# Kernel tuning notes

Hardware: AMD Instinct MI355X
Metric: run time of the kernel (lower is better)

Reference implementation:

```python
import jax, jax.numpy as jnp
from jax import lax
import numpy as np

B, C, T = 32, 62, 1024
SR = 256
NUM_T = 32
POOL, STEP = 16, 4
OUT_G, POOL_G = 64, 32
NUM_CLASS = 4
KS = [int(0.1 * SR), int(0.2 * SR), int(0.5 * SR)]  # 25, 51, 128
EPS = 1e-30

def _feat_size():
    total = 0
    for k in KS:
        L = T - k + 1
        total += (L - POOL) // STEP + 1
    return NUM_T * (total // 2)  # AvgPool(1,2) halves the concat length

F_DIM = _feat_size()  # 32 * 354 = 11328


def setup_inputs() -> dict:
    key = jax.random.key(0)
    ks = jax.random.split(key, 32)
    n = lambda i, shape, s=0.05: jax.random.normal(ks[i], shape, dtype=jnp.float32) * s
    return dict(
        x=jax.random.normal(ks[0], (B, 1, C, T), dtype=jnp.float32),
        conv1_w=n(1, (NUM_T, 1, 1, KS[0])), conv1_b=jnp.zeros((NUM_T,), jnp.float32),
        conv2_w=n(2, (NUM_T, 1, 1, KS[1])), conv2_b=jnp.zeros((NUM_T,), jnp.float32),
        conv3_w=n(3, (NUM_T, 1, 1, KS[2])), conv3_b=jnp.zeros((NUM_T,), jnp.float32),
        oxo_w=n(4, (NUM_T, NUM_T)), oxo_b=jnp.zeros((NUM_T,), jnp.float32),
        lf_w=n(5, (C, F_DIM), 1.0), lf_b=jnp.zeros((1, C, 1), jnp.float32),
        global_adj=n(6, (C, C), 1.0),
        entry_w=n(7, (F_DIM, OUT_G)), entry_b=jnp.zeros((1, 1, OUT_G), jnp.float32),
        pool_w=n(8, (F_DIM, POOL_G)), pool_b=jnp.zeros((1, 1, POOL_G), jnp.float32),
        pl_w=n(9, (POOL_G, POOL_G), 0.1), pl_b=jnp.zeros((POOL_G,), jnp.float32),
        embed_w=n(10, (OUT_G, OUT_G), 0.1), embed_b=jnp.zeros((1, 1, OUT_G), jnp.float32),
        fc1_w=n(11, (2 * OUT_G, 2 * OUT_G), 0.1), fc1_b=jnp.zeros((2 * OUT_G,), jnp.float32),
        fc2_w=n(12, (2 * OUT_G, OUT_G), 0.1), fc2_b=jnp.zeros((OUT_G,), jnp.float32),
        fc3_w=n(13, (OUT_G, NUM_CLASS), 0.1), fc3_b=jnp.zeros((NUM_CLASS,), jnp.float32),
    )


def _bn(t, axes, eps=1e-5):
    # training-mode batchnorm with gamma=1, beta=0 (init values)
    m = t.mean(axes, keepdims=True)
    v = t.var(axes, keepdims=True)
    return (t - m) / jnp.sqrt(v + eps)


def _temporal(x, w, b):
    # Conv2d(1, NUM_T, (1,k)) -> square -> AvgPool(1,POOL) stride (1,STEP) -> log
    y = lax.conv_general_dilated(x, w, (1, 1), 'VALID',
                                 dimension_numbers=('NCHW', 'OIHW', 'NCHW'))
    y = y + b[None, :, None, None]
    y = y * y
    y = lax.reduce_window(y, 0.0, lax.add, (1, 1, 1, POOL), (1, 1, 1, STEP), 'VALID') / POOL
    return jnp.log(y)


def _forward(x, conv1_w, conv1_b, conv2_w, conv2_b, conv3_w, conv3_b, oxo_w, oxo_b,
             lf_w, lf_b, global_adj, entry_w, entry_b, pool_w, pool_b, pl_w, pl_b,
             embed_w, embed_b, fc1_w, fc1_b, fc2_w, fc2_b, fc3_w, fc3_b):
    # temporal branches, concat along time
    out = jnp.concatenate([_temporal(x, conv1_w, conv1_b),
                           _temporal(x, conv2_w, conv2_b),
                           _temporal(x, conv3_w, conv3_b)], axis=-1)  # [B,NUM_T,C,Lt]
    out = _bn(out, (0, 2, 3))  # BN_t
    # OneXOneConv: dropout(eval)=id, 1x1 conv, leaky_relu, AvgPool(1,2)
    out = jnp.einsum('bchw,oc->bohw', out, oxo_w) + oxo_b[None, :, None, None]
    out = jnp.where(out > 0, out, 0.01 * out)
    out = lax.reduce_window(out, 0.0, lax.add, (1, 1, 1, 2), (1, 1, 1, 2), 'VALID') / 2.0
    out = _bn(out, (0, 2, 3))  # BN_t_
    # [B,NUM_T,C,L] -> [B,C,NUM_T*L]
    out = jnp.transpose(out, (0, 2, 1, 3)).reshape(out.shape[0], C, -1)
    # local_filter_fun + apply_bn
    out = jax.nn.relu(out * lf_w[None] - lf_b)
    out = _bn(out, (0, 2))
    # get_adj: self-similarity, learned global adj, self loops, sym normalization
    s = jnp.einsum('bnf,bmf->bnm', out, out)
    adj = jax.nn.relu(s * (global_adj + global_adj.T)) + jnp.eye(C, dtype=out.dtype)
    rowsum = adj.sum(-1)
    rowsum = jnp.where(rowsum == 0, rowsum + 1.0, rowsum)
    d = rowsum ** -0.5
    adj = adj * d[:, :, None] * d[:, None, :]
    # entry GCN + bn_ + attention pooling (softmax over last dim of size 1 -> ones)
    h_entry = _bn(jnp.einsum('bnm,bmf->bnf', adj, out) @ entry_w - entry_b, (0, 2))
    tg1 = jnp.tanh(h_entry.mean(1))
    sc1 = jax.nn.softmax(jnp.einsum('bnf,bf->bn', h_entry, tg1)[..., None], axis=-1)
    rep1 = jnp.einsum('bnf,bn->bf', h_entry, sc1[..., 0])
    # pool GCN -> assignment
    h_pool = _bn(jnp.einsum('bnm,bmf->bnf', adj, out) @ pool_w - pool_b, (0, 2))
    s_assign = jax.nn.softmax(h_pool @ pl_w + pl_b, axis=-1)  # [B,C,POOL_G]
    # dense_diff_pool
    x_pool = jnp.einsum('bnk,bnf->bkf', s_assign, h_entry)
    adj_pool = jnp.einsum('bnk,bnm,bml->bkl', s_assign, adj, s_assign)
    link = adj - jnp.einsum('bnk,bmk->bnm', s_assign, s_assign) + EPS
    link_loss = jnp.linalg.norm(link.reshape(-1)) / adj.size
    ent_loss = (-s_assign * jnp.log(s_assign + EPS)).sum(-1).mean()
    # embed GCN + apply_bn + attention pooling
    h = _bn(jnp.einsum('bkl,blf->bkf', adj_pool, x_pool) @ embed_w - embed_b, (0, 2))
    tg2 = jnp.tanh(h.mean(1))
    sc2 = jax.nn.softmax(jnp.einsum('bkf,bf->bk', h, tg2)[..., None], axis=-1)
    rep2 = jnp.einsum('bkf,bk->bf', h, sc2[..., 0])
    # head
    o = jnp.concatenate([rep1, rep2], axis=1)
    o = jax.nn.relu(o @ fc1_w + fc1_b)
    o = jax.nn.relu(o @ fc2_w + fc2_b)
    o = o @ fc3_w + fc3_b
    o = _bn(o, (0,))  # apply_bn on [B, num_class]
    return o, link_loss, ent_loss


def reference(x, conv1_w, conv1_b, conv2_w, conv2_b, conv3_w, conv3_b, oxo_w, oxo_b,
              lf_w, lf_b, global_adj, entry_w, entry_b, pool_w, pool_b, pl_w, pl_b,
              embed_w, embed_b, fc1_w, fc1_b, fc2_w, fc2_b, fc3_w, fc3_b):
    return _forward(x, conv1_w, conv1_b, conv2_w, conv2_b, conv3_w, conv3_b, oxo_w, oxo_b,
                    lf_w, lf_b, global_adj, entry_w, entry_b, pool_w, pool_b, pl_w, pl_b,
                    embed_w, embed_b, fc1_w, fc1_b, fc2_w, fc2_b, fc3_w, fc3_b)
```

## Files before the change

kernel.cpp:

```cpp
#include <hip/hip_runtime.h>
#include <math.h>

typedef float  f32x4 __attribute__((ext_vector_type(4)));
typedef short  s16x4 __attribute__((ext_vector_type(4)));
typedef short  s16x8 __attribute__((ext_vector_type(8)));

constexpr int cB  = 32;
constexpr int cC  = 62;
constexpr int cT  = 1024;
constexpr int cNT = 32;
constexpr int cLT = 708;
constexpr int cLT2= 354;
constexpr int cFD = 11328;
constexpr int cNBC = cB*cC;

constexpr size_t FEAT_N = (size_t)cB*cNT*cC*cLT;
constexpr size_t P_N    = (size_t)cB*cC*cC;
constexpr size_t Q_N    = (size_t)cB*cC*96;
constexpr size_t R_N    = (size_t)cB*64;
constexpr size_t PART_N = (size_t)cNBC*64;
constexpr size_t ADJ_N  = P_N;
constexpr size_t HE_N   = (size_t)cB*cC*64;
constexpr size_t HP_N   = (size_t)cB*cC*32;
constexpr size_t HPRE_N = (size_t)cB*32*64;
constexpr int WBF_N = 32*32 + 32*64 + 32*128;

__device__ __forceinline__ unsigned short bf16rne(float v){
  unsigned int u = __float_as_uint(v);
  unsigned int r = (u + 0x7fffu + ((u>>16)&1u)) >> 16;
  return (unsigned short)r;
}

__global__ __launch_bounds__(256) void k_prep(
    const float* __restrict__ w1, const float* __restrict__ w2,
    const float* __restrict__ w3, const float* __restrict__ entry_w,
    const float* __restrict__ pool_w,
    unsigned short* __restrict__ wH, unsigned short* __restrict__ wL,
    float* __restrict__ wcol)
{
  int blk = blockIdx.x, tid = threadIdx.x;
  if (blk < 28){
    int i = blk*256 + tid;
    float v;
    if (i < 1024){ int f=i>>5, k=i&31; v = (k<25) ? w1[f*25+k] : 0.f; }
    else if (i < 3072){ int j=i-1024; int f=j>>6, k=j&63; v = (k<51) ? w2[f*51+k] : 0.f; }
    else { v = w3[i-3072]; }
    unsigned short h = bf16rne(v);
    float hf = __uint_as_float(((unsigned int)h)<<16);
    wH[i] = h;
    wL[i] = bf16rne(v - hf);
  } else {
    int j = blk - 28;
    float s = 0.f;
    if (j < 64){ for (int k=tid;k<cFD;k+=256) s += entry_w[(size_t)k*64 + j]; }
    else       { for (int k=tid;k<cFD;k+=256) s += pool_w[(size_t)k*32 + (j-64)]; }
    __shared__ float red[256];
    red[tid]=s; __syncthreads();
    for (int o=128;o>0;o>>=1){ if(tid<o) red[tid]+=red[tid+o]; __syncthreads(); }
    if (tid==0) wcol[j] = red[0];
  }
}

template<int KS, int MT, int WOFF>
__device__ __forceinline__ void mfma_branch(
    const unsigned short* xH, const unsigned short* xL,
    const unsigned short* __restrict__ wHg, const unsigned short* __restrict__ wLg,
    const float* __restrict__ biasg, float* pt, int tid)
{
  int lane = tid & 63, wv = tid >> 6;
  int f = lane & 15, q = lane >> 4;
  int s = lane & 3;
  int a12 = lane & 12;
  s16x8 BH[2][KS], BL[2][KS];
  #pragma unroll
  for (int nt=0; nt<2; nt++)
    #pragma unroll
    for (int ks=0; ks<KS; ks++){
      size_t wo = (size_t)WOFF + (size_t)(nt*16+f)*(KS*32) + ks*32 + q*8;
      BH[nt][ks] = *(const s16x8*)&wHg[wo];
      BL[nt][ks] = *(const s16x8*)&wLg[wo];
    }
  float bv0 = biasg[f], bv1 = biasg[16+f];
  for (int mt = wv; mt < MT; mt += 4){
    f32x4 acc0 = {0.f,0.f,0.f,0.f};
    f32x4 acc1 = {0.f,0.f,0.f,0.f};
    int e0 = mt*16 + a12;
    #pragma unroll
    for (int ks=0; ks<KS; ks++){
      int e = e0 + q*8 + ks*32;
      const unsigned short* ph = xH + s*1160 + e;
      const unsigned short* pl = xL + s*1160 + e;
      s16x4 h0 = *(const s16x4*)ph;
      s16x4 h1 = *(const s16x4*)(ph+4);
      s16x4 l0 = *(const s16x4*)pl;
      s16x4 l1 = *(const s16x4*)(pl+4);
      s16x8 Ah = __builtin_shufflevector(h0,h1,0,1,2,3,4,5,6,7);
      s16x8 Al = __builtin_shufflevector(l0,l1,0,1,2,3,4,5,6,7);
      acc0 = __builtin_amdgcn_mfma_f32_16x16x32_bf16(Ah, BH[0][ks], acc0, 0,0,0);
      acc0 = __builtin_amdgcn_mfma_f32_16x16x32_bf16(Ah, BL[0][ks], acc0, 0,0,0);
      acc0 = __builtin_amdgcn_mfma_f32_16x16x32_bf16(Al, BH[0][ks], acc0, 0,0,0);
      acc1 = __builtin_amdgcn_mfma_f32_16x16x32_bf16(Ah, BH[1][ks], acc1, 0,0,0);
      acc1 = __builtin_amdgcn_mfma_f32_16x16x32_bf16(Ah, BL[1][ks], acc1, 0,0,0);
      acc1 = __builtin_amdgcn_mfma_f32_16x16x32_bf16(Al, BH[1][ks], acc1, 0,0,0);
    }
    float p0=0.f, p1=0.f;
    #pragma unroll
    for (int r=0;r<4;r++){
      float t0 = acc0[r]+bv0; p0 = fmaf(t0,t0,p0);
      float t1 = acc1[r]+bv1; p1 = fmaf(t1,t1,p1);
    }
    pt[(size_t)f*261      + mt*4 + q] = p0;
    pt[(size_t)(16+f)*261 + mt*4 + q] = p1;
  }
}

template<int P, int OFF>
__device__ __forceinline__ void pool_phase(
    const float* pt, float* __restrict__ feat, size_t rstr, size_t base_bc,
    float* tsum, float* tsq, int tid)
{
  bool act = tid < P;
  for (int fi=0; fi<32; fi++){
    float lv = 0.f;
    if (act){
      const float* pp = &pt[(size_t)fi*261 + tid];
      float pooled = (pp[0]+pp[1]+pp[2]+pp[3])*(1.f/16.f);
      lv = __logf(pooled);
      feat[base_bc + (size_t)fi*rstr + OFF + tid] = lv;
    }
    float v = lv, qq = lv*lv;
    #pragma unroll
    for (int o=32;o>0;o>>=1){ v += __shfl_down(v,o,64); qq += __shfl_down(qq,o,64); }
    if ((tid&63)==0){ atomicAdd(&tsum[fi], v); atomicAdd(&tsq[fi], qq); }
  }
}

__global__ __launch_bounds__(256) void k_conv(
    const float* __restrict__ x,
    const unsigned short* __restrict__ wH, const unsigned short* __restrict__ wL,
    const float* __restrict__ b1, const float* __restrict__ b2, const float* __restrict__ b3,
    float* __restrict__ feat, float* __restrict__ part1)
{
  __shared__ unsigned short xH[4*1160];
  __shared__ unsigned short xL[4*1160];
  __shared__ float pt[32*261];
  __shared__ float tsum[32], tsq[32];
  int b = blockIdx.x / cC, c = blockIdx.x % cC;
  int tid = threadIdx.x;
  const float* xg = x + (size_t)(b*cC+c)*cT;
  if (tid<32){ tsum[tid]=0.f; tsq[tid]=0.f; }
  for (int i=tid; i<4*1160; i+=256){
    int s = i / 1160, idx = i - s*1160;
    int src = idx + s;
    float v = (src < 1024) ? xg[src] : 0.f;
    unsigned short h = bf16rne(v);
    float hf = __uint_as_float(((unsigned int)h)<<16);
    xH[i] = h;
    xL[i] = bf16rne(v - hf);
  }
  size_t base_bc = ((size_t)(b*cNT)*cC + c)*cLT;
  size_t rstr = (size_t)cC*cLT;
  __syncthreads();
  mfma_branch<1,63,0>(xH,xL,wH,wL,b1,pt,tid);
  __syncthreads();
  pool_phase<247,0>(pt,feat,rstr,base_bc,tsum,tsq,tid);
  __syncthreads();
  mfma_branch<2,61,1024>(xH,xL,wH,wL,b2,pt,tid);
  __syncthreads();
  pool_phase<240,247>(pt,feat,rstr,base_bc,tsum,tsq,tid);
  __syncthreads();
  mfma_branch<4,57,3072>(xH,xL,wH,wL,b3,pt,tid);
  __syncthreads();
  pool_phase<221,487>(pt,feat,rstr,base_bc,tsum,tsq,tid);
  __syncthreads();
  if (tid<32){
    part1[(size_t)blockIdx.x*64 + tid*2]   = tsum[tid];
    part1[(size_t)blockIdx.x*64 + tid*2+1] = tsq[tid];
  }
}

__global__ __launch_bounds__(256) void k_reduce_stats(
    const float* __restrict__ part, double* __restrict__ stat, int nblk, int nch)
{
  int ch = blockIdx.x, tid = threadIdx.x;
  double s=0,q=0;
  for (int i=tid;i<nblk;i+=256){
    s += (double)part[(size_t)i*nch*2 + ch*2];
    q += (double)part[(size_t)i*nch*2 + ch*2 + 1];
  }
  __shared__ double ls[256], lq[256];
  ls[tid]=s; lq[tid]=q; __syncthreads();
  for (int o=128;o>0;o>>=1){ if(tid<o){ls[tid]+=ls[tid+o]; lq[tid]+=lq[tid+o];} __syncthreads(); }
  if (tid==0){ stat[ch*2]=ls[0]; stat[ch*2+1]=lq[0]; }
}

__global__ void k_foldw(const double* __restrict__ stat1,
                        const float* __restrict__ oxo_w, const float* __restrict__ oxo_b,
                        float* __restrict__ W2T, float* __restrict__ Cf)
{
  __shared__ float mu[32], inv[32];
  int tid = threadIdx.x;
  if (tid<32){
    double cnt = (double)cB*cC*cLT;
    double m = stat1[tid*2]/cnt;
    double v = stat1[tid*2+1]/cnt - m*m;
    mu[tid] = (float)m; inv[tid] = (float)(1.0/sqrt(v+1e-5));
  }
  __syncthreads();
  for (int i=tid;i<1024;i+=256){
    int t=i>>5, o=i&31;
    W2T[t*32+o] = oxo_w[o*32+t]*inv[t];
  }
  if (tid<32){
    float cacc = oxo_b[tid];
    for (int t=0;t<32;t++) cacc -= oxo_w[tid*32+t]*inv[t]*mu[t];
    Cf[tid] = cacc;
  }
}

__global__ __launch_bounds__(256) void k_mix(
    float* __restrict__ feat, const float* __restrict__ W2T,
    const float* __restrict__ Cf, float* __restrict__ part2)
{
  __shared__ float ft[32*240];
  __shared__ float wLh[1024];
  __shared__ float cL[32];
  int b = blockIdx.x / cC, c = blockIdx.x % cC;
  int tid = threadIdx.x;
  int lane = tid & 63, oset = (tid>>6)*8;
  for (int i=tid;i<1024;i+=256) wLh[i] = W2T[i];
  if (tid<32) cL[tid] = Cf[tid];
  float sacc[8]={0,0,0,0,0,0,0,0}, qacc[8]={0,0,0,0,0,0,0,0};
  for (int ch=0; ch<3; ch++){
    int l0 = ch*236;
    __syncthreads();
    for (int g=tid; g<32*59; g+=256){
      int t = g/59, l4 = (g - t*59)*4;
      *(float4*)&ft[t*240+l4] = *(const float4*)&feat[((size_t)(b*cNT+t)*cC + c)*cLT + l0 + l4];
    }
    __syncthreads();
    if (lane < 59){
      float m[8][4];
      #pragma unroll
      for (int f=0;f<8;f++){ float cv=cL[oset+f]; m[f][0]=cv;m[f][1]=cv;m[f][2]=cv;m[f][3]=cv; }
      #pragma unroll 4
      for (int t=0;t<32;t++){
        float4 z = *(const float4*)&ft[t*240 + 4*lane];
        float4 wa = *(const float4*)&wLh[t*32+oset];
        float4 wb = *(const float4*)&wLh[t*32+oset+4];
        float w8a[8] = {wa.x,wa.y,wa.z,wa.w, wb.x,wb.y,wb.z,wb.w};
        #pragma unroll
        for (int f=0;f<8;f++){
          m[f][0]=fmaf(z.x,w8a[f],m[f][0]);
          m[f][1]=fmaf(z.y,w8a[f],m[f][1]);
          m[f][2]=fmaf(z.z,w8a[f],m[f][2]);
          m[f][3]=fmaf(z.w,w8a[f],m[f][3]);
        }
      }
      #pragma unroll
      for (int f=0;f<8;f++){
        float a0 = m[f][0]>0.f ? m[f][0] : 0.01f*m[f][0];
        float a1 = m[f][1]>0.f ? m[f][1] : 0.01f*m[f][1];
        float a2 = m[f][2]>0.f ? m[f][2] : 0.01f*m[f][2];
        float a3 = m[f][3]>0.f ? m[f][3] : 0.01f*m[f][3];
        float v0 = 0.5f*(a0+a1), v1 = 0.5f*(a2+a3);
        float2 st; st.x=v0; st.y=v1;
        *(float2*)&feat[((size_t)(b*cNT+oset+f)*cC + c)*cLT + 118*ch + 2*lane] = st;
        sacc[f] += v0+v1; qacc[f] += v0*v0+v1*v1;
      }
    }
  }
  #pragma unroll
  for (int f=0;f<8;f++){
    float s = sacc[f], q = qacc[f];
    #pragma unroll
    for (int o=32;o>0;o>>=1){ s += __shfl_down(s,o,64); q += __shfl_down(q,o,64); }
    if (lane==0){
      part2[(size_t)blockIdx.x*64 + (oset+f)*2]   = s;
      part2[(size_t)blockIdx.x*64 + (oset+f)*2+1] = q;
    }
  }
}

__global__ __launch_bounds__(256) void k_gramow(
    const float* __restrict__ featbuf, const double* __restrict__ stat2,
    const float* __restrict__ lf_w, const float* __restrict__ lf_b,
    const float* __restrict__ entry_w, const float* __restrict__ pool_w,
    float* __restrict__ P, float* __restrict__ Q, float* __restrict__ r_g)
{
  __shared__ float lt[64*68];
  __shared__ float lw[64*100];
  __shared__ float a_s[32], b_s[32];
  __shared__ float lbs[64];
  int b = blockIdx.x >> 4, ks = blockIdx.x & 15;
  int tid = threadIdx.x;
  if (tid<32){
    double cnt = (double)cB*cC*cLT2;
    double m = stat2[tid*2]/cnt;
    double v = stat2[tid*2+1]/cnt - m*m;
    float inv = (float)(1.0/sqrt(v+1e-5));
    a_s[tid] = inv;
    b_s[tid] = -(float)m * inv;
  }
  if (tid<64) lbs[tid] = (tid<62) ? lf_b[tid] : 0.f;
  float accG[4][4] = {{0.f}};
  float accO[4][6] = {{0.f}};
  float accR[4]    = {0.f,0.f,0.f,0.f};
  int n0 = (tid>>4)<<2;
  int mg = (tid&15)<<2;
  int jo = (tid&15)*6;
  int kk = tid & 63, nr = tid >> 6;
  for (int tile=ks; tile<177; tile+=16){
    int k0 = tile<<6;
    int f = k0 + kk, t = f/cLT2, l2 = f - t*cLT2;
    __syncthreads();
    for (int n=nr; n<64; n+=4){
      float v = 0.f;
      if (n<62){
        float raw = featbuf[((size_t)(b*cNT+t)*cC + n)*cLT + l2];
        float z = fmaf(raw, a_s[t], b_s[t]);
        v = fmaxf(fmaf(z, lf_w[(size_t)n*cFD + f], -lbs[n]), 0.f);
      }
      lt[kk*68 + n] = v;
    }
    for (int i=tid;i<6144;i+=256){
      int kw = i/96, j = i-kw*96;
      float wv = (j<64) ? entry_w[(size_t)(k0+kw)*64 + j] : pool_w[(size_t)(k0+kw)*32 + (j-64)];
      lw[kw*100 + j] = wv;
    }
    __syncthreads();
    #pragma unroll 4
    for (int k=0;k<64;k++){
      const float4 av = *(const float4*)&lt[k*68 + n0];
      const float4 bv = *(const float4*)&lt[k*68 + mg];
      const float2 w0 = *(const float2*)&lw[k*100+jo];
      const float2 w1 = *(const float2*)&lw[k*100+jo+2];
      const float2 w2 = *(const float2*)&lw[k*100+jo+4];
      float avv[4] = {av.x,av.y,av.z,av.w};
      float bvv[4] = {bv.x,bv.y,bv.z,bv.w};
      float wv[6]  = {w0.x,w0.y,w1.x,w1.y,w2.x,w2.y};
      #pragma unroll
      for (int i=0;i<4;i++){
        accR[i] += avv[i];
        #pragma unroll
        for (int j=0;j<4;j++) accG[i][j] = fmaf(avv[i], bvv[j], accG[i][j]);
        #pragma unroll
        for (int j=0;j<6;j++) accO[i][j] = fmaf(avv[i], wv[j], accO[i][j]);
      }
    }
  }
  for (int i=0;i<4;i++) if (n0+i<62){
    for (int j=0;j<4;j++) if (mg+j<62)
      atomicAdd(&P[((size_t)b*cC + n0+i)*cC + mg+j], accG[i][j]);
    for (int j=0;j<6;j++)
      atomicAdd(&Q[((size_t)b*cC + n0+i)*96 + jo+j], accO[i][j]);
  }
  if ((tid&15)==0)
    for (int i=0;i<4;i++) if (n0+i<62)
      atomicAdd(&r_g[(size_t)b*64 + n0+i], accR[i]);
}

__global__ __launch_bounds__(256) void k_adjgcn(
    const float* __restrict__ P, const float* __restrict__ r_g,
    const float* __restrict__ gadj, const float* __restrict__ Q,
    const float* __restrict__ wcol,
    const float* __restrict__ entry_b, const float* __restrict__ pool_b,
    float* __restrict__ adj, float* __restrict__ hE, float* __restrict__ hP,
    double* __restrict__ statE, double* __restrict__ statP)
{
  __shared__ float a[3844];
  __shared__ float oL[5952];
  __shared__ float dsh[62];
  __shared__ float rL[62], mL[62], iL[62], wcL[96];
  __shared__ float es[62], eq[62], ps[62], pq[62];
  int b = blockIdx.x, tid = threadIdx.x;
  if (tid<62){
    double S=0, SQ=0;
    for (int b2=0;b2<32;b2++){
      S  += (double)r_g[(size_t)b2*64 + tid];
      SQ += (double)P[((size_t)b2*cC + tid)*cC + tid];
    }
    double cnt = (double)cB*cFD;
    double m = S/cnt, var = SQ/cnt - m*m;
    mL[tid] = (float)m;
    iL[tid] = (float)(1.0/sqrt(var+1e-5));
    rL[tid] = r_g[(size_t)b*64+tid];
    es[tid]=0.f; eq[tid]=0.f; ps[tid]=0.f; pq[tid]=0.f;
  }
  if (tid>=64 && tid<160) wcL[tid-64]=wcol[tid-64];
  __syncthreads();
  for (int i=tid;i<3844;i+=256){
    int n=i/62, m=i-n*62;
    float sv = (P[(size_t)b*3844+i] - mL[n]*rL[m] - mL[m]*rL[n] + (float)cFD*mL[n]*mL[m]) * iL[n]*iL[m];
    float g = gadj[n*62+m] + gadj[m*62+n];
    float v = sv*g;
    v = v>0.f ? v : 0.f;
    if (n==m) v += 1.f;
    a[i]=v;
  }
  for (int i=tid;i<5952;i+=256){
    int m=i/96, j=i-m*96;
    oL[i] = (Q[(size_t)b*5952+i] - mL[m]*wcL[j]) * iL[m];
  }
  __syncthreads();
  if (tid<62){
    float rsum=0.f;
    for (int m=0;m<62;m++) rsum += a[tid*62+m];
    if (rsum==0.f) rsum=1.f;
    dsh[tid] = 1.0f/sqrtf(rsum);
  }
  __syncthreads();
  for (int i=tid;i<3844;i+=256){
    int n=i/62, m=i-n*62;
    float v = a[i]*dsh[n]*dsh[m];
    a[i] = v;
    adj[(size_t)b*3844+i] = v;
  }
  __syncthreads();
  for (int i=tid;i<5952;i+=256){
    int n=i/96, j=i-n*96;
    float v=0.f;
    for (int m=0;m<62;m++) v = fmaf(a[n*62+m], oL[m*96+j], v);
    if (j<64){
      v -= entry_b[j];
      hE[((size_t)b*62+n)*64 + j] = v;
      atomicAdd(&es[n],v); atomicAdd(&eq[n],v*v);
    } else {
      int j2=j-64;
      v -= pool_b[j2];
      hP[((size_t)b*62+n)*32 + j2] = v;
      atomicAdd(&ps[n],v); atomicAdd(&pq[n],v*v);
    }
  }
  __syncthreads();
  if (tid<62){
    atomicAdd(&statE[tid*2],(double)es[tid]);
    atomicAdd(&statE[tid*2+1],(double)eq[tid]);
    atomicAdd(&statP[tid*2],(double)ps[tid]);
    atomicAdd(&statP[tid*2+1],(double)pq[tid]);
  }
}

__global__ __launch_bounds__(256) void k_pool(
    const float* __restrict__ adj, const float* __restrict__ hEraw,
    const float* __restrict__ hPraw,
    const double* __restrict__ statE, const double* __restrict__ statP,
    const float* __restrict__ pl_w, const float* __restrict__ pl_b,
    const float* __restrict__ embed_w, const float* __restrict__ embed_b,
    float* __restrict__ hpre, double* __restrict__ statH, double* __restrict__ accs)
{
  __shared__ float aL[3844];
  __shared__ float sL[1984];
  __shared__ float hL[3968];
  __shared__ float t1[1984];
  __shared__ float xp[2048];
  __shared__ float ap[1024];
  __shared__ float red[256];
  __shared__ float ksum[32], ksq[32];
  __shared__ float mE[62], iE[62], mP[62], iP[62];
  float* e1 = hL;
  float* sT = t1;
  float* hPL = xp;
  float* plw = ap;
  int b = blockIdx.x, tid = threadIdx.x;
  if (tid<62){
    double cntE = (double)cB*64;
    double m = statE[tid*2]/cntE;
    double v = statE[tid*2+1]/cntE - m*m;
    mE[tid]=(float)m; iE[tid]=(float)(1.0/sqrt(v+1e-5));
    double cntP = (double)cB*32;
    double m2 = statP[tid*2]/cntP;
    double v2 = statP[tid*2+1]/cntP - m2*m2;
    mP[tid]=(float)m2; iP[tid]=(float)(1.0/sqrt(v2+1e-5));
  }
  if (tid<32){ksum[tid]=0.f;ksq[tid]=0.f;}
  for (int i=tid;i<3844;i+=256) aL[i]=adj[(size_t)b*3844+i];
  for (int i=tid;i<1984;i+=256) hPL[i]=hPraw[(size_t)b*1984+i];
  for (int i=tid;i<1024;i+=256) plw[i]=pl_w[i];
  __syncthreads();
  for (int i=tid;i<3968;i+=256){
    int n = i>>6;
    hL[i] = (hEraw[(size_t)b*3968+i]-mE[n])*iE[n];
  }
  int r0 = tid>>5, o = tid&31;
  float entacc = 0.f;
  for (int n=r0; n<62; n+=8){
    float y = pl_b[o];
    float mm = mP[n], ii = iP[n];
    #pragma unroll 8
    for (int j=0;j<32;j++)
      y = fmaf((hPL[n*32+j]-mm)*ii, plw[j*32+o], y);
    float mx = y;
    for (int d=16;d>0;d>>=1) mx = fmaxf(mx, __shfl_xor(mx,d,32));
    float e = expf(y-mx);
    float sum = e;
    for (int d=16;d>0;d>>=1) sum += __shfl_xor(sum,d,32);
    float p = e/sum;
    sL[n*32+o] = p;
    entacc += -p*logf(p+1e-30f);
  }
  red[tid]=entacc; __syncthreads();
  for (int o2=128;o2>0;o2>>=1){ if(tid<o2) red[tid]+=red[tid+o2]; __syncthreads(); }
  if (tid==0) atomicAdd(&accs[1], (double)red[0]);
  __syncthreads();
  for (int i=tid;i<2048;i+=256){
    int k=i>>6, f=i&63;
    float v=0.f;
    for (int n=0;n<62;n++) v = fmaf(sL[n*32+k], hL[n*64+f], v);
    xp[i]=v;
  }
  for (int i=tid;i<1984;i+=256){
    int n=i>>5, k=i&31;
    float v=0.f;
    for (int m=0;m<62;m++) v = fmaf(aL[n*62+m], sL[m*32+k], v);
    t1[i]=v;
  }
  __syncthreads();
  for (int i=tid;i<1024;i+=256){
    int k=i>>5, l=i&31;
    float v=0.f;
    for (int n=0;n<62;n++) v = fmaf(sL[n*32+k], t1[n*32+l], v);
    ap[i]=v;
  }
  __syncthreads();
  for (int i=tid;i<1984;i+=256){
    int k=i/62, n=i-k*62;
    sT[k*62+n] = sL[n*32+k];
  }
  __syncthreads();
  float lacc=0.f;
  for (int i=tid;i<3844;i+=256){
    int n=i/62, m=i-n*62;
    float v=0.f;
    for (int k=0;k<32;k++) v = fmaf(sT[k*62+n], sT[k*62+m], v);
    float d = aL[i]-v+1e-30f;
    lacc = fmaf(d,d,lacc);
  }
  red[tid]=lacc; __syncthreads();
  for (int o2=128;o2>0;o2>>=1){ if(tid<o2) red[tid]+=red[tid+o2]; __syncthreads(); }
  if (tid==0) atomicAdd(&accs[0], (double)red[0]);
  __syncthreads();
  for (int i=tid;i<2048;i+=256){
    int k=i>>6, f=i&63;
    float v=0.f;
    for (int l=0;l<32;l++) v = fmaf(ap[k*32+l], xp[l*64+f], v);
    e1[i]=v;
  }
  __syncthreads();
  for (int i=tid;i<2048;i+=256){
    int k=i>>6, j=i&63;
    float v=0.f;
    for (int f=0;f<64;f++) v = fmaf(e1[k*64+f], embed_w[f*64+j], v);
    v -= embed_b[j];
    hpre[(size_t)b*2048 + i] = v;
    atomicAdd(&ksum[k], v);
    atomicAdd(&ksq[k], v*v);
  }
  __syncthreads();
  if (tid<32){
    atomicAdd(&statH[tid*2],   (double)ksum[tid]);
    atomicAdd(&statH[tid*2+1], (double)ksq[tid]);
  }
}

__global__ __launch_bounds__(128) void k_head(
    const float* __restrict__ hEraw, const float* __restrict__ hpre,
    const double* __restrict__ statE, const double* __restrict__ statH,
    const float* __restrict__ fc1_w, const float* __restrict__ fc1_b,
    const float* __restrict__ fc2_w, const float* __restrict__ fc2_b,
    const float* __restrict__ fc3_w, const float* __restrict__ fc3_b,
    float* __restrict__ o_pre)
{
  __shared__ float o1[128], y1[128], y2[64];
  __shared__ float mk[32], ik[32];
  __shared__ float mE[62], iE[62];
  int b = blockIdx.x, tid = threadIdx.x;
  if (tid<32){
    double cnt = 2048.0;
    double m = statH[tid*2]/cnt;
    double v = statH[tid*2+1]/cnt - m*m;
    mk[tid]=(float)m; ik[tid]=(float)(1.0/sqrt(v+1e-5));
  }
  if (tid>=64 && tid<126){
    int n = tid-64;
    double cnt = (double)cB*64;
    double m = statE[n*2]/cnt;
    double v = statE[n*2+1]/cnt - m*m;
    mE[n]=(float)m; iE[n]=(float)(1.0/sqrt(v+1e-5));
  }
  __syncthreads();
  if (tid<64){
    float s1=0.f;
    for (int n=0;n<62;n++)
      s1 += (hEraw[((size_t)b*62+n)*64+tid]-mE[n])*iE[n];
    o1[tid]=s1;
    float s2=0.f;
    for (int k=0;k<32;k++) s2 += (hpre[(size_t)b*2048 + k*64+tid]-mk[k])*ik[k];
    o1[64+tid]=s2;
  }
  __syncthreads();
  {
    float y = fc1_b[tid];
    for (int j=0;j<128;j++) y = fmaf(o1[j], fc1_w[j*128+tid], y);
    y1[tid] = fmaxf(y,0.f);
  }
  __syncthreads();
  if (tid<64){
    float z = fc2_b[tid];
    for (int j=0;j<128;j++) z = fmaf(y1[j], fc2_w[j*64+tid], z);
    y2[tid]=fmaxf(z,0.f);
  }
  __syncthreads();
  if (tid<4){
    float w = fc3_b[tid];
    for (int j=0;j<64;j++) w = fmaf(y2[j], fc3_w[j*4+tid], w);
    o_pre[b*4+tid]=w;
  }
}

__global__ void k_final(const float* __restrict__ o_pre, const double* __restrict__ accs,
                        float* __restrict__ out)
{
  int tid = threadIdx.x;
  if (tid<4){
    float s=0.f,q=0.f;
    for (int b=0;b<32;b++){ float v=o_pre[b*4+tid]; s+=v; q+=v*v; }
    float m = s*(1.f/32.f);
    float var = q*(1.f/32.f) - m*m;
    float inv = 1.0f/sqrtf(var+1e-5f);
    for (int b=0;b<32;b++) out[b*4+tid] = (o_pre[b*4+tid]-m)*inv;
  }
  if (tid==4) out[128] = (float)(sqrt(accs[0])/123008.0);
  if (tid==5) out[129] = (float)(accs[1]/1984.0);
}

__global__ void k_wsfail(float* __restrict__ out, int n)
{
  int i = blockIdx.x*256 + threadIdx.x;
  if (i < n) out[i] = 12345.0f;
}

extern "C" void kernel_launch(void* const* d_in, const int* in_sizes, int n_in,
                              void* d_out, int out_size, void* d_ws, size_t ws_size,
                              hipStream_t stream)
{
  const float* x       = (const float*)d_in[0];
  const float* w1      = (const float*)d_in[1];
  const float* b1      = (const float*)d_in[2];
  const float* w2      = (const float*)d_in[3];
  const float* b2      = (const float*)d_in[4];
  const float* w3      = (const float*)d_in[5];
  const float* b3      = (const float*)d_in[6];
  const float* oxo_w   = (const float*)d_in[7];
  const float* oxo_b   = (const float*)d_in[8];
  const float* lf_w    = (const float*)d_in[9];
  const float* lf_b    = (const float*)d_in[10];
  const float* gadj    = (const float*)d_in[11];
  const float* entry_w = (const float*)d_in[12];
  const float* entry_b = (const float*)d_in[13];
  const float* pool_w  = (const float*)d_in[14];
  const float* pool_b  = (const float*)d_in[15];
  const float* pl_w    = (const float*)d_in[16];
  const float* pl_b    = (const float*)d_in[17];
  const float* embed_w = (const float*)d_in[18];
  const float* embed_b = (const float*)d_in[19];
  const float* fc1_w   = (const float*)d_in[20];
  const float* fc1_b   = (const float*)d_in[21];
  const float* fc2_w   = (const float*)d_in[22];
  const float* fc2_b   = (const float*)d_in[23];
  const float* fc3_w   = (const float*)d_in[24];
  const float* fc3_b   = (const float*)d_in[25];

  char* ws = (char*)d_ws;
  size_t off = 0;
  auto take = [&](size_t bytes){ size_t o = off; off = (off + bytes + 15) & ~(size_t)15; return o; };

  size_t feat_o = take(FEAT_N*4);
  size_t zstart = off;
  size_t P_o     = take(P_N*4);
  size_t Q_o     = take(Q_N*4);
  size_t r_o     = take(R_N*4);
  size_t statE_o = take(124*8);
  size_t statP_o = take(124*8);
  size_t statH_o = take(64*8);
  size_t accs_o  = take(2*8);
  size_t zend = off;
  size_t stat1_o = take(64*8);
  size_t stat2_o = take(64*8);
  size_t wcol_o  = take(96*4);
  size_t w2t_o   = take(1024*4);
  size_t cf_o    = take(32*4);
  size_t part1_o = take(PART_N*4);
  size_t part2_o = take(PART_N*4);
  size_t adj_o   = take(ADJ_N*4);
  size_t hE_o    = take(HE_N*4);
  size_t hP_o    = take(HP_N*4);
  size_t hpre_o  = take(HPRE_N*4);
  size_t opre_o  = take(128*4);
  size_t wbfH_o  = take(WBF_N*2);
  size_t wbfL_o  = take(WBF_N*2);

  if (off > ws_size) {
    k_wsfail<<<(out_size+255)/256, 256, 0, stream>>>((float*)d_out, out_size);
    return;
  }

  float*  feat  = (float*)(ws+feat_o);
  float*  P_g   = (float*)(ws+P_o);
  float*  Q_g   = (float*)(ws+Q_o);
  float*  r_g   = (float*)(ws+r_o);
  double* statE = (double*)(ws+statE_o);
  double* statP = (double*)(ws+statP_o);
  double* statH = (double*)(ws+statH_o);
  double* accs  = (double*)(ws+accs_o);
  double* stat1 = (double*)(ws+stat1_o);
  double* stat2 = (double*)(ws+stat2_o);
  float*  wcol  = (float*)(ws+wcol_o);
  float*  W2T   = (float*)(ws+w2t_o);
  float*  Cf    = (float*)(ws+cf_o);
  float*  part1 = (float*)(ws+part1_o);
  float*  part2 = (float*)(ws+part2_o);
  float*  adj_g = (float*)(ws+adj_o);
  float*  hE_g  = (float*)(ws+hE_o);
  float*  hP_g  = (float*)(ws+hP_o);
  float*  hpre  = (float*)(ws+hpre_o);
  float*  opre  = (float*)(ws+opre_o);
  unsigned short* wbfH = (unsigned short*)(ws+wbfH_o);
  unsigned short* wbfL = (unsigned short*)(ws+wbfL_o);
  float*  out   = (float*)d_out;

  hipMemsetAsync(ws + zstart, 0, zend - zstart, stream);

  k_prep<<<124, 256, 0, stream>>>(w1, w2, w3, entry_w, pool_w, wbfH, wbfL, wcol);
  k_conv<<<cNBC, 256, 0, stream>>>(x, wbfH, wbfL, b1, b2, b3, feat, part1);
  k_reduce_stats<<<32, 256, 0, stream>>>(part1, stat1, cNBC, 32);
  k_foldw<<<1, 256, 0, stream>>>(stat1, oxo_w, oxo_b, W2T, Cf);
  k_mix<<<cNBC, 256, 0, stream>>>(feat, W2T, Cf, part2);
  k_reduce_stats<<<32, 256, 0, stream>>>(part2, stat2, cNBC, 32);
  k_gramow<<<cB*16, 256, 0, stream>>>(feat, stat2, lf_w, lf_b, entry_w, pool_w, P_g, Q_g, r_g);
  k_adjgcn<<<cB, 256, 0, stream>>>(P_g, r_g, gadj, Q_g, wcol, entry_b, pool_b,
                                   adj_g, hE_g, hP_g, statE, statP);
  k_pool<<<cB, 256, 0, stream>>>(adj_g, hE_g, hP_g, statE, statP, pl_w, pl_b,
                                 embed_w, embed_b, hpre, statH, accs);
  k_head<<<cB, 128, 0, stream>>>(hE_g, hpre, statE, statH, fc1_w, fc1_b, fc2_w, fc2_b, fc3_w, fc3_b, opre);
  k_final<<<1, 64, 0, stream>>>(opre, accs, out);
}
```

Before: 780.6 us.

## Move Gram and weight products onto split-bf16 MFMA with a separate value-prep pass

```diff
diff --git a/kernel.cpp b/kernel.cpp
--- a/kernel.cpp
+++ b/kernel.cpp
@@ -24,6 +24,7 @@
 constexpr size_t HP_N   = (size_t)cB*cC*32;
 constexpr size_t HPRE_N = (size_t)cB*32*64;
 constexpr int WBF_N = 32*32 + 32*64 + 32*128;
+constexpr size_t WT_N = (size_t)96*cFD;
 
 __device__ __forceinline__ unsigned short bf16rne(float v){
   unsigned int u = __float_as_uint(v);
@@ -36,7 +37,8 @@
     const float* __restrict__ w3, const float* __restrict__ entry_w,
     const float* __restrict__ pool_w,
     unsigned short* __restrict__ wH, unsigned short* __restrict__ wL,
-    float* __restrict__ wcol)
+    float* __restrict__ wcol,
+    unsigned short* __restrict__ WTH, unsigned short* __restrict__ WTL)
 {
   int blk = blockIdx.x, tid = threadIdx.x;
   if (blk < 28){
@@ -52,8 +54,14 @@
   } else {
     int j = blk - 28;
     float s = 0.f;
-    if (j < 64){ for (int k=tid;k<cFD;k+=256) s += entry_w[(size_t)k*64 + j]; }
-    else       { for (int k=tid;k<cFD;k+=256) s += pool_w[(size_t)k*32 + (j-64)]; }
+    for (int k=tid;k<cFD;k+=256){
+      float v = (j<64) ? entry_w[(size_t)k*64 + j] : pool_w[(size_t)k*32 + (j-64)];
+      s += v;
+      unsigned short h = bf16rne(v);
+      float hf = __uint_as_float(((unsigned int)h)<<16);
+      WTH[(size_t)j*cFD + k] = h;
+      WTL[(size_t)j*cFD + k] = bf16rne(v - hf);
+    }
     __shared__ float red[256];
     red[tid]=s; __syncthreads();
     for (int o=128;o>0;o>>=1){ if(tid<o) red[tid]+=red[tid+o]; __syncthreads(); }
@@ -282,17 +290,14 @@
   }
 }
 
-__global__ __launch_bounds__(256) void k_gramow(
-    const float* __restrict__ featbuf, const double* __restrict__ stat2,
+__global__ __launch_bounds__(256) void k_vprep(
+    float* __restrict__ feat, const double* __restrict__ stat2,
     const float* __restrict__ lf_w, const float* __restrict__ lf_b,
-    const float* __restrict__ entry_w, const float* __restrict__ pool_w,
-    float* __restrict__ P, float* __restrict__ Q, float* __restrict__ r_g)
-{
-  __shared__ float lt[64*68];
-  __shared__ float lw[64*100];
+    float* __restrict__ r_g, float* __restrict__ SQb)
+{
   __shared__ float a_s[32], b_s[32];
-  __shared__ float lbs[64];
-  int b = blockIdx.x >> 4, ks = blockIdx.x & 15;
+  __shared__ float red[256], red2[256];
+  int b = blockIdx.x / cC, c = blockIdx.x % cC;
   int tid = threadIdx.x;
   if (tid<32){
     double cnt = (double)cB*cC*cLT2;
@@ -300,68 +305,125 @@
     double v = stat2[tid*2+1]/cnt - m*m;
     float inv = (float)(1.0/sqrt(v+1e-5));
     a_s[tid] = inv;
-    b_s[tid] = -(float)m * inv;
-  }
-  if (tid<64) lbs[tid] = (tid<62) ? lf_b[tid] : 0.f;
-  float accG[4][4] = {{0.f}};
-  float accO[4][6] = {{0.f}};
-  float accR[4]    = {0.f,0.f,0.f,0.f};
-  int n0 = (tid>>4)<<2;
-  int mg = (tid&15)<<2;
-  int jo = (tid&15)*6;
-  int kk = tid & 63, nr = tid >> 6;
-  for (int tile=ks; tile<177; tile+=16){
-    int k0 = tile<<6;
-    int f = k0 + kk, t = f/cLT2, l2 = f - t*cLT2;
+    b_s[tid] = -(float)m*inv;
+  }
+  __syncthreads();
+  float lb = lf_b[c];
+  float S=0.f, SQ=0.f;
+  unsigned* featU = (unsigned*)feat;
+  for (int i=tid;i<cFD;i+=256){
+    int t = i/cLT2, l2 = i - t*cLT2;
+    size_t ad = ((size_t)(b*cNT+t)*cC + c)*cLT + l2;
+    float raw = feat[ad];
+    float z = fmaf(raw, a_s[t], b_s[t]);
+    float v = fmaxf(fmaf(z, lf_w[(size_t)c*cFD + i], -lb), 0.f);
+    S += v; SQ = fmaf(v,v,SQ);
+    unsigned short h = bf16rne(v);
+    float hf = __uint_as_float(((unsigned int)h)<<16);
+    unsigned short lo = bf16rne(v - hf);
+    featU[ad] = (((unsigned)h)<<16) | (unsigned)lo;
+  }
+  red[tid]=S; red2[tid]=SQ; __syncthreads();
+  for (int o=128;o>0;o>>=1){ if(tid<o){red[tid]+=red[tid+o]; red2[tid]+=red2[tid+o];} __syncthreads(); }
+  if (tid==0){ r_g[b*64+c]=red[0]; SQb[b*64+c]=red2[0]; }
+}
+
+__global__ __launch_bounds__(256) void k_gram(
+    const unsigned* __restrict__ featP,
+    const unsigned short* __restrict__ WTH, const unsigned short* __restrict__ WTL,
+    float* __restrict__ P, float* __restrict__ Q)
+{
+  __shared__ unsigned short VH[64*72];
+  __shared__ unsigned short VL[64*72];
+  __shared__ unsigned short WH[96*72];
+  __shared__ unsigned short WL[96*72];
+  int b = blockIdx.x >> 4, ks = blockIdx.x & 15;
+  int tid = threadIdx.x;
+  int lane = tid & 63, wv = tid >> 6;
+  int cn = lane & 15, q = lane >> 4;
+  int nts[3]; int nnt = 0;
+  for (int t = wv; t < 10; t += 4) nts[nnt++] = t;
+  f32x4 acc[4][3];
+  #pragma unroll
+  for (int mt=0;mt<4;mt++)
+    #pragma unroll
+    for (int j=0;j<3;j++) acc[mt][j] = (f32x4){0.f,0.f,0.f,0.f};
+
+  int t0 = (ks*64)/cLT2;
+  int l20 = ks*64 - t0*cLT2;
+  for (int chunk = ks; chunk < 177; chunk += 16){
     __syncthreads();
-    for (int n=nr; n<64; n+=4){
-      float v = 0.f;
-      if (n<62){
-        float raw = featbuf[((size_t)(b*cNT+t)*cC + n)*cLT + l2];
-        float z = fmaf(raw, a_s[t], b_s[t]);
-        v = fmaxf(fmaf(z, lf_w[(size_t)n*cFD + f], -lbs[n]), 0.f);
+    for (int i=tid; i<62*64; i+=256){
+      int n = i>>6, k = i&63;
+      int fl = l20 + k;
+      int cross = (fl >= cLT2);
+      int t = t0 + cross;
+      int l2 = fl - (cross ? cLT2 : 0);
+      unsigned w = featP[((size_t)(b*cNT+t)*cC + n)*cLT + l2];
+      VH[n*72+k] = (unsigned short)(w>>16);
+      VL[n*72+k] = (unsigned short)(w & 0xffffu);
+    }
+    {
+      int k0 = chunk*64;
+      for (int i=tid; i<96*64; i+=256){
+        int n = i>>6, k = i&63;
+        WH[n*72+k] = WTH[(size_t)n*cFD + k0 + k];
+        WL[n*72+k] = WTL[(size_t)n*cFD + k0 + k];
       }
-      lt[kk*68 + n] = v;
-    }
-    for (int i=tid;i<6144;i+=256){
-      int kw = i/96, j = i-kw*96;
-      float wv = (j<64) ? entry_w[(size_t)(k0+kw)*64 + j] : pool_w[(size_t)(k0+kw)*32 + (j-64)];
-      lw[kw*100 + j] = wv;
     }
     __syncthreads();
-    #pragma unroll 4
-    for (int k=0;k<64;k++){
-      const float4 av = *(const float4*)&lt[k*68 + n0];
-      const float4 bv = *(const float4*)&lt[k*68 + mg];
-      const float2 w0 = *(const float2*)&lw[k*100+jo];
-      const float2 w1 = *(const float2*)&lw[k*100+jo+2];
-      const float2 w2 = *(const float2*)&lw[k*100+jo+4];
-      float avv[4] = {av.x,av.y,av.z,av.w};
-      float bvv[4] = {bv.x,bv.y,bv.z,bv.w};
-      float wv[6]  = {w0.x,w0.y,w1.x,w1.y,w2.x,w2.y};
+    #pragma unroll
+    for (int kst=0;kst<2;kst++){
+      s16x8 AH[4], AL[4];
       #pragma unroll
-      for (int i=0;i<4;i++){
-        accR[i] += avv[i];
+      for (int mt=0;mt<4;mt++){
+        AH[mt] = *(const s16x8*)&VH[(mt*16+cn)*72 + kst*32 + q*8];
+        AL[mt] = *(const s16x8*)&VL[(mt*16+cn)*72 + kst*32 + q*8];
+      }
+      for (int j=0;j<nnt;j++){
+        int nt = nts[j];
+        s16x8 BH, BL;
+        if (nt < 4){
+          BH = *(const s16x8*)&VH[(nt*16+cn)*72 + kst*32 + q*8];
+          BL = *(const s16x8*)&VL[(nt*16+cn)*72 + kst*32 + q*8];
+        } else {
+          BH = *(const s16x8*)&WH[((nt-4)*16+cn)*72 + kst*32 + q*8];
+          BL = *(const s16x8*)&WL[((nt-4)*16+cn)*72 + kst*32 + q*8];
+        }
         #pragma unroll
-        for (int j=0;j<4;j++) accG[i][j] = fmaf(avv[i], bvv[j], accG[i][j]);
-        #pragma unroll
-        for (int j=0;j<6;j++) accO[i][j] = fmaf(avv[i], wv[j], accO[i][j]);
+        for (int mt=0;mt<4;mt++){
+          acc[mt][j] = __builtin_amdgcn_mfma_f32_16x16x32_bf16(AH[mt], BH, acc[mt][j],0,0,0);
+          acc[mt][j] = __builtin_amdgcn_mfma_f32_16x16x32_bf16(AH[mt], BL, acc[mt][j],0,0,0);
+          acc[mt][j] = __builtin_amdgcn_mfma_f32_16x16x32_bf16(AL[mt], BH, acc[mt][j],0,0,0);
+        }
       }
     }
-  }
-  for (int i=0;i<4;i++) if (n0+i<62){
-    for (int j=0;j<4;j++) if (mg+j<62)
-      atomicAdd(&P[((size_t)b*cC + n0+i)*cC + mg+j], accG[i][j]);
-    for (int j=0;j<6;j++)
-      atomicAdd(&Q[((size_t)b*cC + n0+i)*96 + jo+j], accO[i][j]);
-  }
-  if ((tid&15)==0)
-    for (int i=0;i<4;i++) if (n0+i<62)
-      atomicAdd(&r_g[(size_t)b*64 + n0+i], accR[i]);
+    l20 += 1024;
+    while (l20 >= cLT2){ l20 -= cLT2; t0++; }
+  }
+  for (int j=0;j<nnt;j++){
+    int nt = nts[j];
+    for (int mt=0;mt<4;mt++){
+      #pragma unroll
+      for (int r=0;r<4;r++){
+        int m = mt*16 + q*4 + r;
+        if (m >= 62) continue;
+        float v = acc[mt][j][r];
+        if (nt < 4){
+          int n = nt*16 + cn;
+          if (n < 62) atomicAdd(&P[((size_t)b*cC+m)*cC + n], v);
+        } else {
+          int jn = (nt-4)*16 + cn;
+          atomicAdd(&Q[((size_t)b*cC+m)*96 + jn], v);
+        }
+      }
+    }
+  }
 }
 
 __global__ __launch_bounds__(256) void k_adjgcn(
     const float* __restrict__ P, const float* __restrict__ r_g,
+    const float* __restrict__ SQb,
     const float* __restrict__ gadj, const float* __restrict__ Q,
     const float* __restrict__ wcol,
     const float* __restrict__ entry_b, const float* __restrict__ pool_b,
@@ -378,7 +440,7 @@
     double S=0, SQ=0;
     for (int b2=0;b2<32;b2++){
       S  += (double)r_g[(size_t)b2*64 + tid];
-      SQ += (double)P[((size_t)b2*cC + tid)*cC + tid];
+      SQ += (double)SQb[(size_t)b2*64 + tid];
     }
     double cnt = (double)cB*cFD;
     double m = S/cnt, var = SQ/cnt - m*m;
@@ -680,6 +742,7 @@
   size_t P_o     = take(P_N*4);
   size_t Q_o     = take(Q_N*4);
   size_t r_o     = take(R_N*4);
+  size_t sqb_o   = take(R_N*4);
   size_t statE_o = take(124*8);
   size_t statP_o = take(124*8);
   size_t statH_o = take(64*8);
@@ -699,6 +762,8 @@
   size_t opre_o  = take(128*4);
   size_t wbfH_o  = take(WBF_N*2);
   size_t wbfL_o  = take(WBF_N*2);
+  size_t wtH_o   = take(WT_N*2);
+  size_t wtL_o   = take(WT_N*2);
 
   if (off > ws_size) {
     k_wsfail<<<(out_size+255)/256, 256, 0, stream>>>((float*)d_out, out_size);
@@ -709,6 +774,7 @@
   float*  P_g   = (float*)(ws+P_o);
   float*  Q_g   = (float*)(ws+Q_o);
   float*  r_g   = (float*)(ws+r_o);
+  float*  SQb   = (float*)(ws+sqb_o);
   double* statE = (double*)(ws+statE_o);
   double* statP = (double*)(ws+statP_o);
   double* statH = (double*)(ws+statH_o);
@@ -727,18 +793,21 @@
   float*  opre  = (float*)(ws+opre_o);
   unsigned short* wbfH = (unsigned short*)(ws+wbfH_o);
   unsigned short* wbfL = (unsigned short*)(ws+wbfL_o);
+  unsigned short* WTH  = (unsigned short*)(ws+wtH_o);
+  unsigned short* WTL  = (unsigned short*)(ws+wtL_o);
   float*  out   = (float*)d_out;
 
   hipMemsetAsync(ws + zstart, 0, zend - zstart, stream);
 
-  k_prep<<<124, 256, 0, stream>>>(w1, w2, w3, entry_w, pool_w, wbfH, wbfL, wcol);
+  k_prep<<<124, 256, 0, stream>>>(w1, w2, w3, entry_w, pool_w, wbfH, wbfL, wcol, WTH, WTL);
   k_conv<<<cNBC, 256, 0, stream>>>(x, wbfH, wbfL, b1, b2, b3, feat, part1);
   k_reduce_stats<<<32, 256, 0, stream>>>(part1, stat1, cNBC, 32);
   k_foldw<<<1, 256, 0, stream>>>(stat1, oxo_w, oxo_b, W2T, Cf);
   k_mix<<<cNBC, 256, 0, stream>>>(feat, W2T, Cf, part2);
   k_reduce_stats<<<32, 256, 0, stream>>>(part2, stat2, cNBC, 32);
-  k_gramow<<<cB*16, 256, 0, stream>>>(feat, stat2, lf_w, lf_b, entry_w, pool_w, P_g, Q_g, r_g);
-  k_adjgcn<<<cB, 256, 0, stream>>>(P_g, r_g, gadj, Q_g, wcol, entry_b, pool_b,
+  k_vprep<<<cNBC, 256, 0, stream>>>(feat, stat2, lf_w, lf_b, r_g, SQb);
+  k_gram<<<cB*16, 256, 0, stream>>>((const unsigned*)feat, WTH, WTL, P_g, Q_g);
+  k_adjgcn<<<cB, 256, 0, stream>>>(P_g, r_g, SQb, gadj, Q_g, wcol, entry_b, pool_b,
                                    adj_g, hE_g, hP_g, statE, statP);
   k_pool<<<cB, 256, 0, stream>>>(adj_g, hE_g, hP_g, statE, statP, pl_w, pl_b,
                                  embed_w, embed_b, hpre, statH, accs);
```

Measured after the change: 757.4 us. -3.0%, faster.
